# Kernel tuning notes

Measured on AMD Instinct MI355X. Metric: run time of the kernel, lower is better.

The kernel has to match this reference:

```python
import jax, jax.numpy as jnp
import numpy as np

N = 50000
E = 800000
NFEAT, NHID, NCLASS = 128, 64, 16


def _spmm(row, col, w, x):
    # out[i] = sum_{e: row[e]==i} w[e] * x[col[e]]  -- sparse adj @ x
    return jax.ops.segment_sum(x[col] * w[:, None], row, num_segments=N)


def _gcn_layer(x, row, col, w, W, b):
    return _spmm(row, col, w, x @ W) + b


def setup_inputs() -> dict:
    key = jax.random.key(0)
    ks = jax.random.split(key, 16)
    glorot = lambda k, fi, fo: jax.random.uniform(k, (fi, fo), jnp.float32, -1.0, 1.0) / jnp.sqrt(fi)
    inp = {
        "x": jax.random.normal(ks[0], (N, NFEAT), jnp.float32),
        "edge_row": jax.random.randint(ks[1], (E,), 0, N, jnp.int32),
        "edge_col": jax.random.randint(ks[2], (E,), 0, N, jnp.int32),
        "edge_weight": jax.random.uniform(ks[3], (E,), jnp.float32),
        "W1": glorot(ks[4], NFEAT, NHID), "b1": jnp.zeros((NHID,), jnp.float32),
        "W2": glorot(ks[5], NHID, NHID), "b2": jnp.zeros((NHID,), jnp.float32),
        "W3": glorot(ks[6], NHID, NHID), "b3": jnp.zeros((NHID,), jnp.float32),
        "W4": glorot(ks[7], NHID, NHID), "b4": jnp.zeros((NHID,), jnp.float32),
        "W5": glorot(ks[8], NHID, NCLASS), "b5": jnp.zeros((NCLASS,), jnp.float32),
    }
    return inp


def reference(x, edge_row, edge_col, edge_weight, W1, b1, W2, b2, W3, b3, W4, b4, W5, b5):
    # Inference mode: dropout is identity.
    e1 = _gcn_layer(x, edge_row, edge_col, edge_weight, W1, b1)
    h = jax.nn.relu(e1)
    e2 = _gcn_layer(h, edge_row, edge_col, edge_weight, W2, b2)
    h = jax.nn.relu(e2)
    e3 = _gcn_layer(h, edge_row, edge_col, edge_weight, W3, b3)
    h = jax.nn.relu(e3)
    e4 = _gcn_layer(h, edge_row, edge_col, edge_weight, W4, b4)
    h = jax.nn.relu(e4)
    e5 = _gcn_layer(h, edge_row, edge_col, edge_weight, W5, b5)
    return (jax.nn.log_softmax(e5, axis=1), e1, e2, e3, e4, e5)
```

## Files before the change

kernel.cpp:

```cpp
#include <hip/hip_runtime.h>
#include <math.h>

#define NN 50000
#define NE 800000
#define NFEAT 128
#define NHID 64
#define NCLASS 16
#define NB_SCAN ((NN + 255) / 256)
#define GB ((NN + 63) / 64)
#define SGRP 4
#define ROWS_PER_SGRP ((NN + SGRP - 1) / SGRP)
#define SCHUNKS 392

__device__ inline unsigned short f2bf(float f) {
    unsigned u = __builtin_bit_cast(unsigned, f);
    u += 0x7fffu + ((u >> 16) & 1u);
    return (unsigned short)(u >> 16);
}
__device__ inline float bf2f(unsigned short h) {
    return __builtin_bit_cast(float, (unsigned)h << 16);
}
__device__ inline float pk_w(unsigned v) { return bf2f((unsigned short)(v >> 16)); }
__device__ inline int pk_c(unsigned v) { return (int)(v & 0xffffu); }


__global__ __launch_bounds__(256) void hist_pack_kernel(const int* __restrict__ erow,
                                                        const int* __restrict__ ecol,
                                                        const float* __restrict__ ew,
                                                        int* __restrict__ deg,
                                                        uint2* __restrict__ rr8, int E) {
    int e = blockIdx.x * 256 + threadIdx.x;
    if (e < E) {
        int r = erow[e];
        int k = atomicAdd(&deg[r], 1);
        uint2 v;
        v.x = ((unsigned)r << 16) | (unsigned)k;
        v.y = ((unsigned)f2bf(ew[e]) << 16) | (unsigned)ecol[e];
        rr8[e] = v;
    }
}

__global__ __launch_bounds__(256) void scan_sum_kernel(const int* __restrict__ deg,
                                                       int* __restrict__ blocksum, int n) {
    __shared__ int s[256];
    const int t = threadIdx.x;
    int i = blockIdx.x * 256 + t;
    s[t] = (i < n) ? deg[i] : 0;
    __syncthreads();
#pragma unroll
    for (int off = 128; off > 0; off >>= 1) {
        if (t < off) s[t] += s[t + off];
        __syncthreads();
    }
    if (t == 0) blocksum[blockIdx.x] = s[0];
}

__global__ __launch_bounds__(256) void scan_final_kernel(const int* __restrict__ deg,
                                                         const int* __restrict__ blocksum,
                                                         int* __restrict__ row_ptr, int n) {
    __shared__ int bs[256];
    __shared__ int s[256];
    const int t = threadIdx.x;
    bs[t] = (t < NB_SCAN) ? blocksum[t] : 0;
    __syncthreads();
    for (int off = 1; off < 256; off <<= 1) {
        int u = (t >= off) ? bs[t - off] : 0;
        __syncthreads();
        bs[t] += u;
        __syncthreads();
    }
    const int blockpre = (blockIdx.x == 0) ? 0 : bs[blockIdx.x - 1];

    int i = blockIdx.x * 256 + t;
    int d = (i < n) ? deg[i] : 0;
    s[t] = d;
    __syncthreads();
    for (int off = 1; off < 256; off <<= 1) {
        int u = (t >= off) ? s[t - off] : 0;
        __syncthreads();
        s[t] += u;
        __syncthreads();
    }
    int excl = blockpre + s[t] - d;
    if (i < n) {
        row_ptr[i] = excl;
        if (i == n - 1) row_ptr[n] = excl + d;
    }
}

__global__ __launch_bounds__(256) void scatter_rank8_kernel(const uint2* __restrict__ rr8,
                                                            const int* __restrict__ row_ptr,
                                                            unsigned* __restrict__ pk, int E) {
    const int g = blockIdx.x & (SGRP - 1);
    const int chunk = blockIdx.x / SGRP;
    const int CH = (E + SCHUNKS - 1) / SCHUNKS;
    const int lo = chunk * CH;
    const int hi = (lo + CH < E) ? lo + CH : E;
    const int rlo = g * ROWS_PER_SGRP;
    const int rhi = (rlo + ROWS_PER_SGRP < NN) ? rlo + ROWS_PER_SGRP : NN;
    for (int e = lo + threadIdx.x; e < hi; e += 256) {
        uint2 v = rr8[e];
        int r = (int)(v.x >> 16);
        if (r >= rlo && r < rhi) {
            pk[row_ptr[r] + (int)(v.x & 0xffffu)] = v.y;
        }
    }
}

template <int K, bool RELU_IN>
__global__ __launch_bounds__(256) void gemm64_kernel(const float* __restrict__ in,
                                                     const float* __restrict__ Wg,
                                                     unsigned short* __restrict__ outb, int M) {
    constexpr int KC = 64;
    __shared__ float xs[KC][68];
    __shared__ float Ws[KC][64];
    const int t = threadIdx.x;
    const int tx = t % 16;
    const int ty = t / 16;
    const int r0 = blockIdx.x * 64;

    float acc[4][4];
#pragma unroll
    for (int i = 0; i < 4; i++)
#pragma unroll
        for (int j = 0; j < 4; j++) acc[i][j] = 0.f;

    for (int k0 = 0; k0 < K; k0 += KC) {
        for (int i = t * 4; i < KC * 64; i += 1024) {
            *(float4*)&Ws[i / 64][i % 64] = *(const float4*)&Wg[(size_t)k0 * 64 + i];
        }
        {
            const int r = t / 4;
            const int q = t % 4;
            const int gr = r0 + r;
#pragma unroll
            for (int i = 0; i < 4; i++) {
                int k = q * 16 + i * 4;
                float4 v;
                if (gr < M)
                    v = *(const float4*)&in[(size_t)gr * K + k0 + k];
                else
                    v = make_float4(0.f, 0.f, 0.f, 0.f);
                if (RELU_IN) {
                    v.x = fmaxf(v.x, 0.f);
                    v.y = fmaxf(v.y, 0.f);
                    v.z = fmaxf(v.z, 0.f);
                    v.w = fmaxf(v.w, 0.f);
                }
                xs[k + 0][r] = v.x;
                xs[k + 1][r] = v.y;
                xs[k + 2][r] = v.z;
                xs[k + 3][r] = v.w;
            }
        }
        __syncthreads();
#pragma unroll 8
        for (int k = 0; k < KC; k++) {
            float4 xv = *(const float4*)&xs[k][ty * 4];
            float4 wv = *(const float4*)&Ws[k][tx * 4];
            acc[0][0] += xv.x * wv.x; acc[0][1] += xv.x * wv.y;
            acc[0][2] += xv.x * wv.z; acc[0][3] += xv.x * wv.w;
            acc[1][0] += xv.y * wv.x; acc[1][1] += xv.y * wv.y;
            acc[1][2] += xv.y * wv.z; acc[1][3] += xv.y * wv.w;
            acc[2][0] += xv.z * wv.x; acc[2][1] += xv.z * wv.y;
            acc[2][2] += xv.z * wv.z; acc[2][3] += xv.z * wv.w;
            acc[3][0] += xv.w * wv.x; acc[3][1] += xv.w * wv.y;
            acc[3][2] += xv.w * wv.z; acc[3][3] += xv.w * wv.w;
        }
        __syncthreads();
    }
#pragma unroll
    for (int i = 0; i < 4; i++) {
        int r = r0 + ty * 4 + i;
        if (r < M) {
            ushort4 u;
            u.x = f2bf(acc[i][0]);
            u.y = f2bf(acc[i][1]);
            u.z = f2bf(acc[i][2]);
            u.w = f2bf(acc[i][3]);
            *(ushort4*)&outb[(size_t)r * 64 + tx * 4] = u;
        }
    }
}

template <int NOUT>
__global__ __launch_bounds__(512) void spmm64_fused_kernel(
    const unsigned short* __restrict__ gb,
    const int* __restrict__ row_ptr,
    const unsigned* __restrict__ pk,
    const float* __restrict__ bias,
    const float* __restrict__ Wn,
    float* __restrict__ e_out,
    unsigned short* __restrict__ nxt,
    int M) {
    __shared__ float Wlt[NOUT][65];
    __shared__ float xs[8][64];
    const int t = threadIdx.x;

    for (int idx = t; idx < 64 * NOUT; idx += 512) {
        int k = idx / NOUT, j = idx % NOUT;
        Wlt[j][k] = Wn[idx];
    }

    const int wv = __builtin_amdgcn_readfirstlane(t >> 6);
    const int lane = t & 63;
    const int h = lane >> 5;
    const int f = (lane & 31) * 2;
    int r = blockIdx.x * 8 + wv;
    if (r >= M) r = M - 1;

    float a0 = 0.f, a1 = 0.f;
    int e = row_ptr[r];
    const int end = row_ptr[r + 1];
    for (; e + 16 <= end; e += 16) {
        unsigned q0 = pk[e + 0 + h], q1 = pk[e + 2 + h], q2 = pk[e + 4 + h], q3 = pk[e + 6 + h];
        unsigned q4 = pk[e + 8 + h], q5 = pk[e + 10 + h], q6 = pk[e + 12 + h], q7 = pk[e + 14 + h];
        unsigned g0 = *(const unsigned*)&gb[(size_t)pk_c(q0) * 64 + f];
        unsigned g1 = *(const unsigned*)&gb[(size_t)pk_c(q1) * 64 + f];
        unsigned g2 = *(const unsigned*)&gb[(size_t)pk_c(q2) * 64 + f];
        unsigned g3 = *(const unsigned*)&gb[(size_t)pk_c(q3) * 64 + f];
        unsigned g4 = *(const unsigned*)&gb[(size_t)pk_c(q4) * 64 + f];
        unsigned g5 = *(const unsigned*)&gb[(size_t)pk_c(q5) * 64 + f];
        unsigned g6 = *(const unsigned*)&gb[(size_t)pk_c(q6) * 64 + f];
        unsigned g7 = *(const unsigned*)&gb[(size_t)pk_c(q7) * 64 + f];
        float w;
        w = pk_w(q0); a0 += w * bf2f((unsigned short)(g0 & 0xffffu)); a1 += w * bf2f((unsigned short)(g0 >> 16));
        w = pk_w(q1); a0 += w * bf2f((unsigned short)(g1 & 0xffffu)); a1 += w * bf2f((unsigned short)(g1 >> 16));
        w = pk_w(q2); a0 += w * bf2f((unsigned short)(g2 & 0xffffu)); a1 += w * bf2f((unsigned short)(g2 >> 16));
        w = pk_w(q3); a0 += w * bf2f((unsigned short)(g3 & 0xffffu)); a1 += w * bf2f((unsigned short)(g3 >> 16));
        w = pk_w(q4); a0 += w * bf2f((unsigned short)(g4 & 0xffffu)); a1 += w * bf2f((unsigned short)(g4 >> 16));
        w = pk_w(q5); a0 += w * bf2f((unsigned short)(g5 & 0xffffu)); a1 += w * bf2f((unsigned short)(g5 >> 16));
        w = pk_w(q6); a0 += w * bf2f((unsigned short)(g6 & 0xffffu)); a1 += w * bf2f((unsigned short)(g6 >> 16));
        w = pk_w(q7); a0 += w * bf2f((unsigned short)(g7 & 0xffffu)); a1 += w * bf2f((unsigned short)(g7 >> 16));
    }
    for (; e + 2 <= end; e += 2) {
        unsigned q = pk[e + h];
        unsigned g = *(const unsigned*)&gb[(size_t)pk_c(q) * 64 + f];
        float w = pk_w(q);
        a0 += w * bf2f((unsigned short)(g & 0xffffu));
        a1 += w * bf2f((unsigned short)(g >> 16));
    }
    if (e < end && h == 0) {
        unsigned q = pk[e];
        unsigned g = *(const unsigned*)&gb[(size_t)pk_c(q) * 64 + f];
        float w = pk_w(q);
        a0 += w * bf2f((unsigned short)(g & 0xffffu));
        a1 += w * bf2f((unsigned short)(g >> 16));
    }
    a0 += __shfl_xor(a0, 32);
    a1 += __shfl_xor(a1, 32);
    float2 v;
    v.x = a0 + bias[f];
    v.y = a1 + bias[f + 1];
    if (h == 0) {
        *(float2*)&e_out[(size_t)r * 64 + f] = v;
        xs[wv][f] = fmaxf(v.x, 0.f);
        xs[wv][f + 1] = fmaxf(v.y, 0.f);
    }
    __syncthreads();

    if (NOUT == 64) {
        const int rr = t >> 6;
        const int j = t & 63;
        float acc = 0.f;
#pragma unroll 16
        for (int k = 0; k < 64; k++) acc += xs[rr][k] * Wlt[j][k];
        int gr = blockIdx.x * 8 + rr;
        if (gr < M) nxt[(size_t)gr * 64 + j] = f2bf(acc);
    } else {
        if (t < 8 * NOUT) {
            const int rr = t / NOUT;
            const int j = t % NOUT;
            float acc = 0.f;
#pragma unroll 16
            for (int k = 0; k < 64; k++) acc += xs[rr][k] * Wlt[j][k];
            int gr = blockIdx.x * 8 + rr;
            if (gr < M) nxt[(size_t)gr * NOUT + j] = f2bf(acc);
        }
    }
}

__global__ __launch_bounds__(256) void spmm16_lsm_kernel(const unsigned short* __restrict__ tmpc,
                                                         const int* __restrict__ row_ptr,
                                                         const unsigned* __restrict__ pk,
                                                         const float* __restrict__ bias,
                                                         float* __restrict__ e5,
                                                         float* __restrict__ out0, int M) {
    const int t = threadIdx.x;
    const int wv = __builtin_amdgcn_readfirstlane(t >> 6);
    const int lane = t & 63;
    const int f = lane & 15;
    const int s = lane >> 4;
    const int r = blockIdx.x * 4 + wv;
    if (r >= M) return;

    int e = row_ptr[r];
    const int end = row_ptr[r + 1];
    float acc = 0.f;
    for (; e + 8 <= end; e += 8) {
        unsigned qa = pk[e + s];
        unsigned qb = pk[e + 4 + s];
        acc += pk_w(qa) * bf2f(tmpc[(size_t)pk_c(qa) * 16 + f]);
        acc += pk_w(qb) * bf2f(tmpc[(size_t)pk_c(qb) * 16 + f]);
    }
    if (e + 4 <= end) {
        unsigned q = pk[e + s];
        acc += pk_w(q) * bf2f(tmpc[(size_t)pk_c(q) * 16 + f]);
        e += 4;
    }
    if (s < end - e) {
        unsigned q = pk[e + s];
        acc += pk_w(q) * bf2f(tmpc[(size_t)pk_c(q) * 16 + f]);
    }
    acc += __shfl_xor(acc, 16);
    acc += __shfl_xor(acc, 32);
    float v = acc + bias[f];

    float m = v;
#pragma unroll
    for (int off = 1; off < 16; off <<= 1) m = fmaxf(m, __shfl_xor(m, off, 16));
    float sum = expf(v - m);
#pragma unroll
    for (int off = 1; off < 16; off <<= 1) sum += __shfl_xor(sum, off, 16);
    float ls = logf(sum);
    if (lane < 16) {
        e5[(size_t)r * 16 + f] = v;
        out0[(size_t)r * 16 + f] = v - m - ls;
    }
}


extern "C" void kernel_launch(void* const* d_in, const int* in_sizes, int n_in,
                              void* d_out, int out_size, void* d_ws, size_t ws_size,
                              hipStream_t stream) {
    const float* x = (const float*)d_in[0];
    const int* erow = (const int*)d_in[1];
    const int* ecol = (const int*)d_in[2];
    const float* ew = (const float*)d_in[3];
    const float* W1 = (const float*)d_in[4];
    const float* b1 = (const float*)d_in[5];
    const float* W2 = (const float*)d_in[6];
    const float* b2 = (const float*)d_in[7];
    const float* W3 = (const float*)d_in[8];
    const float* b3 = (const float*)d_in[9];
    const float* W4 = (const float*)d_in[10];
    const float* b4 = (const float*)d_in[11];
    const float* W5 = (const float*)d_in[12];
    const float* b5 = (const float*)d_in[13];

    float* out0 = (float*)d_out;
    float* e1 = out0 + (size_t)NN * NCLASS;
    float* e2 = e1 + (size_t)NN * NHID;
    float* e3 = e2 + (size_t)NN * NHID;
    float* e4 = e3 + (size_t)NN * NHID;
    float* e5 = e4 + (size_t)NN * NHID;

    char* ws = (char*)d_ws;
    unsigned short* tmpA = (unsigned short*)ws; ws += (size_t)NN * NHID * 2;
    unsigned short* tmpB = (unsigned short*)ws; ws += (size_t)NN * NHID * 2;
    unsigned short* tmpc = (unsigned short*)ws; ws += ((size_t)NN * NCLASS * 2 + 255) / 256 * 256;
    int* deg = (int*)ws;      ws += ((size_t)NN * 4 + 255) / 256 * 256;
    int* row_ptr = (int*)ws;  ws += ((size_t)(NN + 1) * 4 + 255) / 256 * 256;
    int* blocksum = (int*)ws; ws += ((size_t)NB_SCAN * 4 + 255) / 256 * 256;
    uint2* rr8 = (uint2*)ws;  ws += (size_t)NE * 8;
    unsigned* pk = (unsigned*)ws; ws += (size_t)NE * 4;

    hipMemsetAsync(deg, 0, (size_t)NN * 4, stream);
    hist_pack_kernel<<<(NE + 255) / 256, 256, 0, stream>>>(erow, ecol, ew, deg, rr8, NE);
    scan_sum_kernel<<<NB_SCAN, 256, 0, stream>>>(deg, blocksum, NN);
    scan_final_kernel<<<NB_SCAN, 256, 0, stream>>>(deg, blocksum, row_ptr, NN);
    scatter_rank8_kernel<<<SGRP * SCHUNKS, 256, 0, stream>>>(rr8, row_ptr, pk, NE);

    gemm64_kernel<NFEAT, false><<<GB, 256, 0, stream>>>(x, W1, tmpA, NN);

    const int FG = NN / 8;
    spmm64_fused_kernel<64><<<FG, 512, 0, stream>>>(tmpA, row_ptr, pk, b1, W2, e1, tmpB, NN);
    spmm64_fused_kernel<64><<<FG, 512, 0, stream>>>(tmpB, row_ptr, pk, b2, W3, e2, tmpA, NN);
    spmm64_fused_kernel<64><<<FG, 512, 0, stream>>>(tmpA, row_ptr, pk, b3, W4, e3, tmpB, NN);
    spmm64_fused_kernel<16><<<FG, 512, 0, stream>>>(tmpB, row_ptr, pk, b4, W5, e4, tmpc, NN);

    spmm16_lsm_kernel<<<(NN + 3) / 4, 256, 0, stream>>>(tmpc, row_ptr, pk, b5, e5, out0, NN);
}
```

Measured before the change: 380.4 us.

## Map one row per half-wave in fused SpMM, halving block size to 256 threads

The fused SpMM+GEMM kernel drops from 512 threads with one wavefront per row, where two half-waves split the edges and are joined by a shuffle. It now uses 256 threads with 32 lanes per row, each row's half-wave walking all of its edges alone. This removes the cross-half reduction and halves the thread count per block. The dense follow-up GEMM has each thread compute two output rows so one shared-memory weight read serves both. Per-row serial edge chains become twice as long, so less memory-level parallelism is exposed per row, and the M bounds checks are removed because NN divides evenly by 8.

```diff
diff --git a/kernel.cpp b/kernel.cpp
--- a/kernel.cpp
+++ b/kernel.cpp
@@ -184,7 +184,7 @@
 }
 
 template <int NOUT>
-__global__ __launch_bounds__(512) void spmm64_fused_kernel(
+__global__ __launch_bounds__(256) void spmm64_fused_kernel(
     const unsigned short* __restrict__ gb,
     const int* __restrict__ row_ptr,
     const unsigned* __restrict__ pk,
@@ -197,76 +197,72 @@
     __shared__ float xs[8][64];
     const int t = threadIdx.x;
 
-    for (int idx = t; idx < 64 * NOUT; idx += 512) {
+    for (int idx = t; idx < 64 * NOUT; idx += 256) {
         int k = idx / NOUT, j = idx % NOUT;
         Wlt[j][k] = Wn[idx];
     }
 
-    const int wv = __builtin_amdgcn_readfirstlane(t >> 6);
-    const int lane = t & 63;
-    const int h = lane >> 5;
-    const int f = (lane & 31) * 2;
-    int r = blockIdx.x * 8 + wv;
-    if (r >= M) r = M - 1;
-
-    float a0 = 0.f, a1 = 0.f;
+    const int rb = t >> 5;
+    const int f2 = (t & 31) * 2;
+    const int r = blockIdx.x * 8 + rb;
+
     int e = row_ptr[r];
     const int end = row_ptr[r + 1];
-    for (; e + 16 <= end; e += 16) {
-        unsigned q0 = pk[e + 0 + h], q1 = pk[e + 2 + h], q2 = pk[e + 4 + h], q3 = pk[e + 6 + h];
-        unsigned q4 = pk[e + 8 + h], q5 = pk[e + 10 + h], q6 = pk[e + 12 + h], q7 = pk[e + 14 + h];
-        unsigned g0 = *(const unsigned*)&gb[(size_t)pk_c(q0) * 64 + f];
-        unsigned g1 = *(const unsigned*)&gb[(size_t)pk_c(q1) * 64 + f];
-        unsigned g2 = *(const unsigned*)&gb[(size_t)pk_c(q2) * 64 + f];
-        unsigned g3 = *(const unsigned*)&gb[(size_t)pk_c(q3) * 64 + f];
-        unsigned g4 = *(const unsigned*)&gb[(size_t)pk_c(q4) * 64 + f];
-        unsigned g5 = *(const unsigned*)&gb[(size_t)pk_c(q5) * 64 + f];
-        unsigned g6 = *(const unsigned*)&gb[(size_t)pk_c(q6) * 64 + f];
-        unsigned g7 = *(const unsigned*)&gb[(size_t)pk_c(q7) * 64 + f];
-        float w;
-        w = pk_w(q0); a0 += w * bf2f((unsigned short)(g0 & 0xffffu)); a1 += w * bf2f((unsigned short)(g0 >> 16));
-        w = pk_w(q1); a0 += w * bf2f((unsigned short)(g1 & 0xffffu)); a1 += w * bf2f((unsigned short)(g1 >> 16));
-        w = pk_w(q2); a0 += w * bf2f((unsigned short)(g2 & 0xffffu)); a1 += w * bf2f((unsigned short)(g2 >> 16));
-        w = pk_w(q3); a0 += w * bf2f((unsigned short)(g3 & 0xffffu)); a1 += w * bf2f((unsigned short)(g3 >> 16));
-        w = pk_w(q4); a0 += w * bf2f((unsigned short)(g4 & 0xffffu)); a1 += w * bf2f((unsigned short)(g4 >> 16));
-        w = pk_w(q5); a0 += w * bf2f((unsigned short)(g5 & 0xffffu)); a1 += w * bf2f((unsigned short)(g5 >> 16));
-        w = pk_w(q6); a0 += w * bf2f((unsigned short)(g6 & 0xffffu)); a1 += w * bf2f((unsigned short)(g6 >> 16));
-        w = pk_w(q7); a0 += w * bf2f((unsigned short)(g7 & 0xffffu)); a1 += w * bf2f((unsigned short)(g7 >> 16));
-    }
-    for (; e + 2 <= end; e += 2) {
-        unsigned q = pk[e + h];
-        unsigned g = *(const unsigned*)&gb[(size_t)pk_c(q) * 64 + f];
-        float w = pk_w(q);
-        a0 += w * bf2f((unsigned short)(g & 0xffffu));
-        a1 += w * bf2f((unsigned short)(g >> 16));
-    }
-    if (e < end && h == 0) {
+    float a0 = 0.f, a1 = 0.f;
+    for (; e + 7 < end; e += 8) {
+        unsigned q0 = pk[e + 0], q1 = pk[e + 1], q2 = pk[e + 2], q3 = pk[e + 3];
+        unsigned q4 = pk[e + 4], q5 = pk[e + 5], q6 = pk[e + 6], q7 = pk[e + 7];
+        unsigned g0 = *(const unsigned*)&gb[(size_t)pk_c(q0) * 64 + f2];
+        unsigned g1 = *(const unsigned*)&gb[(size_t)pk_c(q1) * 64 + f2];
+        unsigned g2 = *(const unsigned*)&gb[(size_t)pk_c(q2) * 64 + f2];
+        unsigned g3 = *(const unsigned*)&gb[(size_t)pk_c(q3) * 64 + f2];
+        unsigned g4 = *(const unsigned*)&gb[(size_t)pk_c(q4) * 64 + f2];
+        unsigned g5 = *(const unsigned*)&gb[(size_t)pk_c(q5) * 64 + f2];
+        unsigned g6 = *(const unsigned*)&gb[(size_t)pk_c(q6) * 64 + f2];
+        unsigned g7 = *(const unsigned*)&gb[(size_t)pk_c(q7) * 64 + f2];
+        a0 += pk_w(q0) * bf2f((unsigned short)(g0 & 0xffffu));
+        a1 += pk_w(q0) * bf2f((unsigned short)(g0 >> 16));
+        a0 += pk_w(q1) * bf2f((unsigned short)(g1 & 0xffffu));
+        a1 += pk_w(q1) * bf2f((unsigned short)(g1 >> 16));
+        a0 += pk_w(q2) * bf2f((unsigned short)(g2 & 0xffffu));
+        a1 += pk_w(q2) * bf2f((unsigned short)(g2 >> 16));
+        a0 += pk_w(q3) * bf2f((unsigned short)(g3 & 0xffffu));
+        a1 += pk_w(q3) * bf2f((unsigned short)(g3 >> 16));
+        a0 += pk_w(q4) * bf2f((unsigned short)(g4 & 0xffffu));
+        a1 += pk_w(q4) * bf2f((unsigned short)(g4 >> 16));
+        a0 += pk_w(q5) * bf2f((unsigned short)(g5 & 0xffffu));
+        a1 += pk_w(q5) * bf2f((unsigned short)(g5 >> 16));
+        a0 += pk_w(q6) * bf2f((unsigned short)(g6 & 0xffffu));
+        a1 += pk_w(q6) * bf2f((unsigned short)(g6 >> 16));
+        a0 += pk_w(q7) * bf2f((unsigned short)(g7 & 0xffffu));
+        a1 += pk_w(q7) * bf2f((unsigned short)(g7 >> 16));
+    }
+    for (; e < end; e++) {
         unsigned q = pk[e];
-        unsigned g = *(const unsigned*)&gb[(size_t)pk_c(q) * 64 + f];
-        float w = pk_w(q);
-        a0 += w * bf2f((unsigned short)(g & 0xffffu));
-        a1 += w * bf2f((unsigned short)(g >> 16));
-    }
-    a0 += __shfl_xor(a0, 32);
-    a1 += __shfl_xor(a1, 32);
+        unsigned g = *(const unsigned*)&gb[(size_t)pk_c(q) * 64 + f2];
+        a0 += pk_w(q) * bf2f((unsigned short)(g & 0xffffu));
+        a1 += pk_w(q) * bf2f((unsigned short)(g >> 16));
+    }
     float2 v;
-    v.x = a0 + bias[f];
-    v.y = a1 + bias[f + 1];
-    if (h == 0) {
-        *(float2*)&e_out[(size_t)r * 64 + f] = v;
-        xs[wv][f] = fmaxf(v.x, 0.f);
-        xs[wv][f + 1] = fmaxf(v.y, 0.f);
-    }
+    v.x = a0 + bias[f2];
+    v.y = a1 + bias[f2 + 1];
+    *(float2*)&e_out[(size_t)r * 64 + f2] = v;
+    xs[rb][f2] = fmaxf(v.x, 0.f);
+    xs[rb][f2 + 1] = fmaxf(v.y, 0.f);
     __syncthreads();
 
     if (NOUT == 64) {
-        const int rr = t >> 6;
+        const int rblk = t >> 6;
         const int j = t & 63;
-        float acc = 0.f;
+        float acc0 = 0.f, acc1 = 0.f;
 #pragma unroll 16
-        for (int k = 0; k < 64; k++) acc += xs[rr][k] * Wlt[j][k];
-        int gr = blockIdx.x * 8 + rr;
-        if (gr < M) nxt[(size_t)gr * 64 + j] = f2bf(acc);
+        for (int k = 0; k < 64; k++) {
+            float w = Wlt[j][k];
+            acc0 += xs[rblk][k] * w;
+            acc1 += xs[rblk + 4][k] * w;
+        }
+        nxt[(size_t)(blockIdx.x * 8 + rblk) * 64 + j] = f2bf(acc0);
+        nxt[(size_t)(blockIdx.x * 8 + rblk + 4) * 64 + j] = f2bf(acc1);
     } else {
         if (t < 8 * NOUT) {
             const int rr = t / NOUT;
@@ -274,8 +270,7 @@
             float acc = 0.f;
 #pragma unroll 16
             for (int k = 0; k < 64; k++) acc += xs[rr][k] * Wlt[j][k];
-            int gr = blockIdx.x * 8 + rr;
-            if (gr < M) nxt[(size_t)gr * NOUT + j] = f2bf(acc);
+            nxt[(size_t)(blockIdx.x * 8 + rr) * NOUT + j] = f2bf(acc);
         }
     }
 }
@@ -374,10 +369,10 @@
     gemm64_kernel<NFEAT, false><<<GB, 256, 0, stream>>>(x, W1, tmpA, NN);
 
     const int FG = NN / 8;
-    spmm64_fused_kernel<64><<<FG, 512, 0, stream>>>(tmpA, row_ptr, pk, b1, W2, e1, tmpB, NN);
-    spmm64_fused_kernel<64><<<FG, 512, 0, stream>>>(tmpB, row_ptr, pk, b2, W3, e2, tmpA, NN);
-    spmm64_fused_kernel<64><<<FG, 512, 0, stream>>>(tmpA, row_ptr, pk, b3, W4, e3, tmpB, NN);
-    spmm64_fused_kernel<16><<<FG, 512, 0, stream>>>(tmpB, row_ptr, pk, b4, W5, e4, tmpc, NN);
+    spmm64_fused_kernel<64><<<FG, 256, 0, stream>>>(tmpA, row_ptr, pk, b1, W2, e1, tmpB, NN);
+    spmm64_fused_kernel<64><<<FG, 256, 0, stream>>>(tmpB, row_ptr, pk, b2, W3, e2, tmpA, NN);
+    spmm64_fused_kernel<64><<<FG, 256, 0, stream>>>(tmpA, row_ptr, pk, b3, W4, e3, tmpB, NN);
+    spmm64_fused_kernel<16><<<FG, 256, 0, stream>>>(tmpB, row_ptr, pk, b4, W5, e4, tmpc, NN);
 
     spmm16_lsm_kernel<<<(NN + 3) / 4, 256, 0, stream>>>(tmpc, row_ptr, pk, b5, e5, out0, NN);
 }
```

Measured after the change: 348.2 us. 8.5% less time.
